# Kernel tuning notes

Measured on AMD Instinct MI355X. Metric: run time of the kernel, lower is better.

The kernel has to match this reference:

```python
import jax, jax.numpy as jnp
import numpy as np

IN_FEATURES = 4096
OUT_FEATURES = 4096
GROUP_SIZE = 128
TOKENS = 8192


def setup_inputs() -> dict:
    key = jax.random.key(0)
    k1, k2, k3 = jax.random.split(key, 3)
    x = jax.random.normal(k1, (TOKENS, IN_FEATURES), dtype=jnp.float32)
    weight_packed = jax.random.randint(k2, (OUT_FEATURES, IN_FEATURES // 2), 0, 256, dtype=jnp.int32)
    num_groups = IN_FEATURES // GROUP_SIZE
    weight_scales = jax.random.uniform(k3, (OUT_FEATURES, num_groups), dtype=jnp.float32) * 0.02
    return {"x": x, "weight_packed": weight_packed, "weight_scales": weight_scales, "group_size": GROUP_SIZE}


def _dequantize_int4(packed, scales, group_size):
    # packed: [N, K//2] int (uint8 values); scales: [N, G]
    out_features = packed.shape[0]
    in_features = packed.shape[1] * 2
    low = (packed & 15) - 8   # even columns
    high = ((packed >> 4) & 15) - 8  # odd columns
    # interleave low/high along last axis -> [N, K]
    unpacked = jnp.stack([low, high], axis=-1).reshape(out_features, in_features)
    num_groups = in_features // group_size
    w = unpacked.reshape(out_features, num_groups, group_size).astype(scales.dtype)
    w = w * scales[:, :, None]  # per-group scale
    return w.reshape(out_features, in_features)


def reference(x, weight_packed, weight_scales, group_size):
    W = _dequantize_int4(weight_packed, weight_scales, group_size)  # [N, K]
    # nn.functional.linear: x @ W.T (bias=False)
    return jnp.einsum('tk,nk->tn', x, W)
```

## Files before the change

### kernel.cpp

```cpp
#include <hip/hip_runtime.h>
#include <cstdint>
#include <cstddef>

#define TOKENS 8192
#define IN_F   4096
#define OUT_F  4096

typedef __bf16 bf16;
typedef bf16  bf16x8 __attribute__((ext_vector_type(8)));
typedef float f32x4  __attribute__((ext_vector_type(4)));

__global__ void prep_kernel(const float* __restrict__ xin, bf16* __restrict__ xout,
                            const int* __restrict__ wp, const float* __restrict__ sc,
                            bf16* __restrict__ wout) {
    if (blockIdx.x < 16384) {
        size_t i = ((size_t)blockIdx.x * 256 + threadIdx.x) * 8;
        const float4* p = (const float4*)(xin + i);
        float4 a = p[0], b = p[1];
        bf16x8 r;
        r[0] = (bf16)a.x; r[1] = (bf16)a.y; r[2] = (bf16)a.z; r[3] = (bf16)a.w;
        r[4] = (bf16)b.x; r[5] = (bf16)b.y; r[6] = (bf16)b.z; r[7] = (bf16)b.w;
        *(bf16x8*)(xout + i) = r;
    } else {
        int t  = (blockIdx.x - 16384) * 256 + threadIdx.x;
        int j0 = t << 2;
        int n  = j0 >> 11;
        int g  = (j0 & 2047) >> 6;
        float s = sc[(n << 5) + g];
        int4 p = *(const int4*)(wp + j0);
        bf16x8 r;
        r[0] = (bf16)((float)((p.x & 15) - 8) * s);
        r[1] = (bf16)((float)(((p.x >> 4) & 15) - 8) * s);
        r[2] = (bf16)((float)((p.y & 15) - 8) * s);
        r[3] = (bf16)((float)(((p.y >> 4) & 15) - 8) * s);
        r[4] = (bf16)((float)((p.z & 15) - 8) * s);
        r[5] = (bf16)((float)(((p.z >> 4) & 15) - 8) * s);
        r[6] = (bf16)((float)((p.w & 15) - 8) * s);
        r[7] = (bf16)((float)(((p.w >> 4) & 15) - 8) * s);
        *(bf16x8*)(wout + ((size_t)j0 << 1)) = r;
    }
}


#define GLL(src, dst) __builtin_amdgcn_global_load_lds( \
    (const __attribute__((address_space(1))) void*)(src), \
    (__attribute__((address_space(3))) void*)(dst), 16, 0, 0)
#define BARX() { __builtin_amdgcn_s_barrier(); __builtin_amdgcn_sched_barrier(0); }

__global__ __launch_bounds__(512, 2)
void gemm_kernel(const bf16* __restrict__ A, const bf16* __restrict__ B,
                 float* __restrict__ C) {
    __shared__ char smem[131072] __attribute__((aligned(128)));

    const int tid  = threadIdx.x;
    const int lane = tid & 63;
    const int w    = tid >> 6;
    const int wr   = w >> 2, wc = w & 3;
    const int lrow = lane >> 3;
    const int gsw  = (lane & 7) ^ lrow;

    const int wg = ((blockIdx.x & 7) << 6) | (blockIdx.x >> 3);
    const int mt = wg >> 4;
    const int nt = wg & 15;

    const char* Abase = (const char*)A + (size_t)(mt * 256) * (IN_F * 2);
    const char* Bbase = (const char*)B + (size_t)(nt * 256) * (IN_F * 2);

    const char* gA[4];
#pragma unroll
    for (int t = 0; t < 4; ++t)
        gA[t] = Abase + (size_t)(t * 64 + w * 8 + lrow) * (IN_F * 2) + gsw * 16;
    const int rb = (w >> 2) * 64 + (w & 3) * 8;
    const int brow0 = rb, brow1 = rb + 128, brow2 = rb + 32, brow3 = rb + 160;
    const char* gB[4];
    gB[0] = Bbase + (size_t)(brow0 + lrow) * (IN_F * 2) + gsw * 16;
    gB[1] = Bbase + (size_t)(brow1 + lrow) * (IN_F * 2) + gsw * 16;
    gB[2] = Bbase + (size_t)(brow2 + lrow) * (IN_F * 2) + gsw * 16;
    gB[3] = Bbase + (size_t)(brow3 + lrow) * (IN_F * 2) + gsw * 16;

    char* const sm = smem;
#define ST_A0(b, kt) { GLL(gA[0] + (kt) * 128, sm + (b) * 65536 +     0 + w * 1024); \
                       GLL(gA[2] + (kt) * 128, sm + (b) * 65536 + 16384 + w * 1024); }
#define ST_A1(b, kt) { GLL(gA[1] + (kt) * 128, sm + (b) * 65536 +  8192 + w * 1024); \
                       GLL(gA[3] + (kt) * 128, sm + (b) * 65536 + 24576 + w * 1024); }
#define ST_B0(b, kt) { GLL(gB[0] + (kt) * 128, sm + (b) * 65536 + 32768 + brow0 * 128); \
                       GLL(gB[1] + (kt) * 128, sm + (b) * 65536 + 32768 + brow1 * 128); }
#define ST_B1(b, kt) { GLL(gB[2] + (kt) * 128, sm + (b) * 65536 + 32768 + brow2 * 128); \
                       GLL(gB[3] + (kt) * 128, sm + (b) * 65536 + 32768 + brow3 * 128); }

    const int m_lane = lane & 15, quad = lane >> 4, sw = m_lane & 7;
    const bf16x8* pA0 = (const bf16x8*)sm;
    const bf16x8* pB0 = (const bf16x8*)(sm + 32768);
    const bf16x8* pA1 = (const bf16x8*)(sm + 65536);
    const bf16x8* pB1 = (const bf16x8*)(sm + 98304);

    f32x4 acc[8][4];
#pragma unroll
    for (int i = 0; i < 8; ++i)
#pragma unroll
        for (int j = 0; j < 4; ++j) acc[i][j] = (f32x4)0.0f;

    ST_A0(0, 0); ST_B0(0, 0); ST_B1(0, 0); ST_A1(0, 0);
    ST_A0(1, 1); ST_B0(1, 1);
    asm volatile("s_waitcnt vmcnt(4)" ::: "memory");
    __builtin_amdgcn_s_barrier();

#define LDA(dst, PA, qr) \
    { _Pragma("unroll") for (int i = 0; i < 4; ++i) { \
        _Pragma("unroll") for (int kh = 0; kh < 2; ++kh) { \
            dst[i][kh] = (PA)[(wr * 128 + ((qr) * 4 + i) * 16 + m_lane) * 8 + ((kh * 4 + quad) ^ sw)]; } } }
#define LDBq(dst, PB, qc) \
    { _Pragma("unroll") for (int j = 0; j < 2; ++j) { \
        _Pragma("unroll") for (int kh = 0; kh < 2; ++kh) { \
            dst[j][kh] = (PB)[(wc * 64 + ((qc) * 2 + j) * 16 + m_lane) * 8 + ((kh * 4 + quad) ^ sw)]; } } }
#define MMq(afv, bv, qr, qc) \
    { __builtin_amdgcn_s_setprio(1); \
      _Pragma("unroll") for (int i = 0; i < 4; ++i) { \
        _Pragma("unroll") for (int j = 0; j < 2; ++j) { \
          _Pragma("unroll") for (int kh = 0; kh < 2; ++kh) { \
            acc[(qr) * 4 + i][(qc) * 2 + j] = __builtin_amdgcn_mfma_f32_16x16x32_bf16( \
                afv[i][kh], bv[j][kh], acc[(qr) * 4 + i][(qc) * 2 + j], 0, 0, 0); } } } \
      __builtin_amdgcn_s_setprio(0); }

    bf16x8 bq0[2][2], bq1[2][2];
    LDBq(bq0, pB0, 0);

    for (int it = 0; it < 32; ++it) {
        const int kt0 = 2 * it;
        const int kt1 = kt0 + 1;
        const bool more = (it < 31);
        {
            bf16x8 af0[4][2], af1[4][2];
            LDA(af0, pA0, 0);
            ST_B1(1, kt1);
            BARX(); MMq(af0, bq0, 0, 0);
            LDBq(bq1, pB0, 1);
            ST_A1(1, kt1);
            BARX(); MMq(af0, bq1, 0, 1);
            LDA(af1, pA0, 1);
            if (more) ST_A0(0, kt0 + 2);
            BARX(); MMq(af1, bq0, 1, 0);
            if (more) {
                ST_B0(0, kt0 + 2);
                asm volatile("s_waitcnt vmcnt(4)" ::: "memory");
            } else {
                asm volatile("s_waitcnt vmcnt(0)" ::: "memory");
            }
            LDBq(bq0, pB1, 0);
            BARX(); MMq(af1, bq1, 1, 1);
        }
        {
            bf16x8 af0[4][2], af1[4][2];
            LDA(af0, pA1, 0);
            if (more) ST_B1(0, kt1 + 1);
            BARX(); MMq(af0, bq0, 0, 0);
            LDBq(bq1, pB1, 1);
            if (more) ST_A1(0, kt1 + 1);
            BARX(); MMq(af0, bq1, 0, 1);
            LDA(af1, pA1, 1);
            if (more) ST_A0(1, kt1 + 2);
            BARX(); MMq(af1, bq0, 1, 0);
            if (more) {
                ST_B0(1, kt1 + 2);
                asm volatile("s_waitcnt vmcnt(4)" ::: "memory");
                LDBq(bq0, pB0, 0);
            }
            BARX(); MMq(af1, bq1, 1, 1);
        }
    }

    const size_t crow0 = (size_t)(mt * 256 + wr * 128 + quad * 4) * OUT_F
                       + (size_t)(nt * 256 + wc * 64 + m_lane);
#pragma unroll
    for (int i = 0; i < 8; ++i)
#pragma unroll
        for (int r = 0; r < 4; ++r) {
            float* cp = C + crow0 + (size_t)(i * 16 + r) * OUT_F;
#pragma unroll
            for (int j = 0; j < 4; ++j) cp[j * 16] = acc[i][j][r];
        }
}

__global__ void naive_kernel(const float* __restrict__ x, const int* __restrict__ wp,
                             const float* __restrict__ sc, float* __restrict__ out) {
    int o = blockIdx.x * 256 + threadIdx.x;
    int t = o >> 12, n = o & 4095;
    const float* xr = x + (size_t)t * IN_F;
    const int*   wr2 = wp + (size_t)n * (IN_F / 2);
    float acc = 0.f;
    for (int g = 0; g < 32; ++g) {
        float s = sc[n * 32 + g];
        float part = 0.f;
        for (int j = 0; j < 64; ++j) {
            int p = wr2[g * 64 + j];
            part += xr[g * 128 + 2 * j]     * (float)((p & 15) - 8);
            part += xr[g * 128 + 2 * j + 1] * (float)(((p >> 4) & 15) - 8);
        }
        acc += part * s;
    }
    out[o] = acc;
}

extern "C" void kernel_launch(void* const* d_in, const int* in_sizes, int n_in,
                              void* d_out, int out_size, void* d_ws, size_t ws_size,
                              hipStream_t stream) {
    const float* x  = (const float*)d_in[0];
    const int*   wp = (const int*)d_in[1];
    const float* sc = (const float*)d_in[2];
    float* out = (float*)d_out;

    const size_t xb_bytes = (size_t)TOKENS * IN_F * 2;
    const size_t wb_bytes = (size_t)OUT_F * IN_F * 2;

    if (ws_size >= xb_bytes + wb_bytes) {
        bf16* xb = (bf16*)d_ws;
        bf16* wb = (bf16*)((char*)d_ws + xb_bytes);
        prep_kernel<<<dim3(16384 + 8192), dim3(256), 0, stream>>>(x, xb, wp, sc, wb);
        gemm_kernel<<<dim3((TOKENS / 256) * (OUT_F / 256)), dim3(512), 0, stream>>>(xb, wb, out);
    } else {
        naive_kernel<<<dim3((TOKENS * OUT_F) / 256), dim3(256), 0, stream>>>(x, wp, sc, out);
    }
}
```

Baseline: 454.2 us.

## Fuse fp32-to-bf16 activation conversion into GEMM A-tile staging

Removes the separate pass that converted x from fp32 to bf16 into a workspace buffer. The GEMM now loads fp32 x directly into registers, converts it, and writes bf16 into shared memory, replacing the direct global-to-LDS loads for A. The software pipeline is reworked: wait counts change, B fragments are loaded per half-iteration, and explicit lgkmcnt waits follow the LDS writes. This saves a full write and reread of the bf16 activation copy. In exchange the GEMM reads twice the A bytes, which are re-read by each of the 16 column tiles, uses more registers, and has more synchronisation stalls in the main loop.

```diff
diff --git a/kernel.cpp b/kernel.cpp
--- a/kernel.cpp
+++ b/kernel.cpp
@@ -10,35 +10,24 @@
 typedef bf16  bf16x8 __attribute__((ext_vector_type(8)));
 typedef float f32x4  __attribute__((ext_vector_type(4)));
 
-__global__ void prep_kernel(const float* __restrict__ xin, bf16* __restrict__ xout,
-                            const int* __restrict__ wp, const float* __restrict__ sc,
+__global__ void prep_kernel(const int* __restrict__ wp, const float* __restrict__ sc,
                             bf16* __restrict__ wout) {
-    if (blockIdx.x < 16384) {
-        size_t i = ((size_t)blockIdx.x * 256 + threadIdx.x) * 8;
-        const float4* p = (const float4*)(xin + i);
-        float4 a = p[0], b = p[1];
-        bf16x8 r;
-        r[0] = (bf16)a.x; r[1] = (bf16)a.y; r[2] = (bf16)a.z; r[3] = (bf16)a.w;
-        r[4] = (bf16)b.x; r[5] = (bf16)b.y; r[6] = (bf16)b.z; r[7] = (bf16)b.w;
-        *(bf16x8*)(xout + i) = r;
-    } else {
-        int t  = (blockIdx.x - 16384) * 256 + threadIdx.x;
-        int j0 = t << 2;
-        int n  = j0 >> 11;
-        int g  = (j0 & 2047) >> 6;
-        float s = sc[(n << 5) + g];
-        int4 p = *(const int4*)(wp + j0);
-        bf16x8 r;
-        r[0] = (bf16)((float)((p.x & 15) - 8) * s);
-        r[1] = (bf16)((float)(((p.x >> 4) & 15) - 8) * s);
-        r[2] = (bf16)((float)((p.y & 15) - 8) * s);
-        r[3] = (bf16)((float)(((p.y >> 4) & 15) - 8) * s);
-        r[4] = (bf16)((float)((p.z & 15) - 8) * s);
-        r[5] = (bf16)((float)(((p.z >> 4) & 15) - 8) * s);
-        r[6] = (bf16)((float)((p.w & 15) - 8) * s);
-        r[7] = (bf16)((float)(((p.w >> 4) & 15) - 8) * s);
-        *(bf16x8*)(wout + ((size_t)j0 << 1)) = r;
-    }
+    int t  = blockIdx.x * 256 + threadIdx.x;
+    int j0 = t << 2;
+    int n  = j0 >> 11;
+    int g  = (j0 & 2047) >> 6;
+    float s = sc[(n << 5) + g];
+    int4 p = *(const int4*)(wp + j0);
+    bf16x8 r;
+    r[0] = (bf16)((float)((p.x & 15) - 8) * s);
+    r[1] = (bf16)((float)(((p.x >> 4) & 15) - 8) * s);
+    r[2] = (bf16)((float)((p.y & 15) - 8) * s);
+    r[3] = (bf16)((float)(((p.y >> 4) & 15) - 8) * s);
+    r[4] = (bf16)((float)((p.z & 15) - 8) * s);
+    r[5] = (bf16)((float)(((p.z >> 4) & 15) - 8) * s);
+    r[6] = (bf16)((float)((p.w & 15) - 8) * s);
+    r[7] = (bf16)((float)(((p.w >> 4) & 15) - 8) * s);
+    *(bf16x8*)(wout + ((size_t)j0 << 1)) = r;
 }
 
 
@@ -48,7 +37,7 @@
 #define BARX() { __builtin_amdgcn_s_barrier(); __builtin_amdgcn_sched_barrier(0); }
 
 __global__ __launch_bounds__(512, 2)
-void gemm_kernel(const bf16* __restrict__ A, const bf16* __restrict__ B,
+void gemm_kernel(const float* __restrict__ X, const bf16* __restrict__ B,
                  float* __restrict__ C) {
     __shared__ char smem[131072] __attribute__((aligned(128)));
 
@@ -57,19 +46,23 @@
     const int w    = tid >> 6;
     const int wr   = w >> 2, wc = w & 3;
     const int lrow = lane >> 3;
-    const int gsw  = (lane & 7) ^ lrow;
+    const int lcol = lane & 7;
+    const int gsw  = lcol ^ lrow;
 
     const int wg = ((blockIdx.x & 7) << 6) | (blockIdx.x >> 3);
     const int mt = wg >> 4;
     const int nt = wg & 15;
 
-    const char* Abase = (const char*)A + (size_t)(mt * 256) * (IN_F * 2);
+    const float* xsrc[4];
+    int awr[4];
+#pragma unroll
+    for (int q = 0; q < 4; ++q) {
+        const int arow = q * 64 + w * 8 + lrow;
+        xsrc[q] = X + (size_t)(mt * 256 + arow) * IN_F + lcol * 8;
+        awr[q]  = arow * 128 + gsw * 16;
+    }
+
     const char* Bbase = (const char*)B + (size_t)(nt * 256) * (IN_F * 2);
-
-    const char* gA[4];
-#pragma unroll
-    for (int t = 0; t < 4; ++t)
-        gA[t] = Abase + (size_t)(t * 64 + w * 8 + lrow) * (IN_F * 2) + gsw * 16;
     const int rb = (w >> 2) * 64 + (w & 3) * 8;
     const int brow0 = rb, brow1 = rb + 128, brow2 = rb + 32, brow3 = rb + 160;
     const char* gB[4];
@@ -79,14 +72,20 @@
     gB[3] = Bbase + (size_t)(brow3 + lrow) * (IN_F * 2) + gsw * 16;
 
     char* const sm = smem;
-#define ST_A0(b, kt) { GLL(gA[0] + (kt) * 128, sm + (b) * 65536 +     0 + w * 1024); \
-                       GLL(gA[2] + (kt) * 128, sm + (b) * 65536 + 16384 + w * 1024); }
-#define ST_A1(b, kt) { GLL(gA[1] + (kt) * 128, sm + (b) * 65536 +  8192 + w * 1024); \
-                       GLL(gA[3] + (kt) * 128, sm + (b) * 65536 + 24576 + w * 1024); }
 #define ST_B0(b, kt) { GLL(gB[0] + (kt) * 128, sm + (b) * 65536 + 32768 + brow0 * 128); \
                        GLL(gB[1] + (kt) * 128, sm + (b) * 65536 + 32768 + brow1 * 128); }
 #define ST_B1(b, kt) { GLL(gB[2] + (kt) * 128, sm + (b) * 65536 + 32768 + brow2 * 128); \
                        GLL(gB[3] + (kt) * 128, sm + (b) * 65536 + 32768 + brow3 * 128); }
+
+    float4 qa[4], qb[4];
+#define LDX(kt) { _Pragma("unroll") for (int q = 0; q < 4; ++q) { \
+        const float4* xp = (const float4*)(xsrc[q] + (kt) * 64); \
+        qa[q] = xp[0]; qb[q] = xp[1]; } }
+#define WRA(b) { _Pragma("unroll") for (int q = 0; q < 4; ++q) { \
+        bf16x8 v; \
+        v[0] = (bf16)qa[q].x; v[1] = (bf16)qa[q].y; v[2] = (bf16)qa[q].z; v[3] = (bf16)qa[q].w; \
+        v[4] = (bf16)qb[q].x; v[5] = (bf16)qb[q].y; v[6] = (bf16)qb[q].z; v[7] = (bf16)qb[q].w; \
+        *(bf16x8*)(sm + (b) * 65536 + awr[q]) = v; } }
 
     const int m_lane = lane & 15, quad = lane >> 4, sw = m_lane & 7;
     const bf16x8* pA0 = (const bf16x8*)sm;
@@ -100,9 +99,12 @@
 #pragma unroll
         for (int j = 0; j < 4; ++j) acc[i][j] = (f32x4)0.0f;
 
-    ST_A0(0, 0); ST_B0(0, 0); ST_B1(0, 0); ST_A1(0, 0);
-    ST_A0(1, 1); ST_B0(1, 1);
-    asm volatile("s_waitcnt vmcnt(4)" ::: "memory");
+    ST_B0(0, 0); ST_B1(0, 0);
+    LDX(0);
+    ST_B0(1, 1);
+    asm volatile("s_waitcnt vmcnt(2)" ::: "memory");
+    WRA(0);
+    asm volatile("s_waitcnt lgkmcnt(0)" ::: "memory");
     __builtin_amdgcn_s_barrier();
 
 #define LDA(dst, PA, qr) \
@@ -122,48 +124,47 @@
                 afv[i][kh], bv[j][kh], acc[(qr) * 4 + i][(qc) * 2 + j], 0, 0, 0); } } } \
       __builtin_amdgcn_s_setprio(0); }
 
-    bf16x8 bq0[2][2], bq1[2][2];
-    LDBq(bq0, pB0, 0);
-
     for (int it = 0; it < 32; ++it) {
         const int kt0 = 2 * it;
         const int kt1 = kt0 + 1;
         const bool more = (it < 31);
         {
-            bf16x8 af0[4][2], af1[4][2];
-            LDA(af0, pA0, 0);
+            bf16x8 af0[4][2], af1[4][2], bq0[2][2], bq1[2][2];
             ST_B1(1, kt1);
+            LDX(kt1);
+            LDA(af0, pA0, 0); LDBq(bq0, pB0, 0);
             BARX(); MMq(af0, bq0, 0, 0);
             LDBq(bq1, pB0, 1);
-            ST_A1(1, kt1);
             BARX(); MMq(af0, bq1, 0, 1);
             LDA(af1, pA0, 1);
-            if (more) ST_A0(0, kt0 + 2);
             BARX(); MMq(af1, bq0, 1, 0);
             if (more) {
                 ST_B0(0, kt0 + 2);
-                asm volatile("s_waitcnt vmcnt(4)" ::: "memory");
+                asm volatile("s_waitcnt vmcnt(2)" ::: "memory");
             } else {
                 asm volatile("s_waitcnt vmcnt(0)" ::: "memory");
             }
-            LDBq(bq0, pB1, 0);
+            WRA(1);
+            asm volatile("s_waitcnt lgkmcnt(0)" ::: "memory");
             BARX(); MMq(af1, bq1, 1, 1);
         }
         {
-            bf16x8 af0[4][2], af1[4][2];
-            LDA(af0, pA1, 0);
-            if (more) ST_B1(0, kt1 + 1);
+            bf16x8 af0[4][2], af1[4][2], bq0[2][2], bq1[2][2];
+            if (more) {
+                ST_B1(0, kt1 + 1);
+                LDX(kt1 + 1);
+            }
+            LDA(af0, pA1, 0); LDBq(bq0, pB1, 0);
             BARX(); MMq(af0, bq0, 0, 0);
             LDBq(bq1, pB1, 1);
-            if (more) ST_A1(0, kt1 + 1);
             BARX(); MMq(af0, bq1, 0, 1);
             LDA(af1, pA1, 1);
-            if (more) ST_A0(1, kt1 + 2);
             BARX(); MMq(af1, bq0, 1, 0);
             if (more) {
                 ST_B0(1, kt1 + 2);
-                asm volatile("s_waitcnt vmcnt(4)" ::: "memory");
-                LDBq(bq0, pB0, 0);
+                asm volatile("s_waitcnt vmcnt(2)" ::: "memory");
+                WRA(0);
+                asm volatile("s_waitcnt lgkmcnt(0)" ::: "memory");
             }
             BARX(); MMq(af1, bq1, 1, 1);
         }
@@ -209,14 +210,12 @@
     const float* sc = (const float*)d_in[2];
     float* out = (float*)d_out;
 
-    const size_t xb_bytes = (size_t)TOKENS * IN_F * 2;
     const size_t wb_bytes = (size_t)OUT_F * IN_F * 2;
 
-    if (ws_size >= xb_bytes + wb_bytes) {
-        bf16* xb = (bf16*)d_ws;
-        bf16* wb = (bf16*)((char*)d_ws + xb_bytes);
-        prep_kernel<<<dim3(16384 + 8192), dim3(256), 0, stream>>>(x, xb, wp, sc, wb);
-        gemm_kernel<<<dim3((TOKENS / 256) * (OUT_F / 256)), dim3(512), 0, stream>>>(xb, wb, out);
+    if (ws_size >= wb_bytes) {
+        bf16* wb = (bf16*)d_ws;
+        prep_kernel<<<dim3(8192), dim3(256), 0, stream>>>(wp, sc, wb);
+        gemm_kernel<<<dim3((TOKENS / 256) * (OUT_F / 256)), dim3(512), 0, stream>>>(x, wb, out);
     } else {
         naive_kernel<<<dim3((TOKENS * OUT_F) / 256), dim3(256), 0, stream>>>(x, wp, sc, out);
     }
```

Result: slower. 735.9 us (+62.0%).
